# Kernel tuning notes

Hardware: AMD Instinct MI355X
Metric: run time of the kernel (lower is better)

The kernel has to match this reference:

```python
import jax, jax.numpy as jnp
import numpy as np

EMBED_DIM = 1024
NUM_HEADS = 16
HEAD_DIM = EMBED_DIM // NUM_HEADS
SCALE = HEAD_DIM ** -0.5
BATCH, SEQ = 2, 2048


def setup_inputs() -> dict:
    key = jax.random.key(0)
    k1, k2, k3 = jax.random.split(key, 3)
    # Xavier-uniform-like init scales
    s_qkv = (6.0 / (3 * EMBED_DIM + EMBED_DIM)) ** 0.5
    s_out = (6.0 / (2 * EMBED_DIM)) ** 0.5
    return {
        "x": jax.random.normal(k1, (BATCH, SEQ, EMBED_DIM), dtype=jnp.float32),
        "w_qkv": jax.random.uniform(k2, (3 * EMBED_DIM, EMBED_DIM), jnp.float32, -s_qkv, s_qkv),
        "w_out": jax.random.uniform(k3, (EMBED_DIM, EMBED_DIM), jnp.float32, -s_out, s_out),
        "bias_qkv": jnp.zeros((3 * EMBED_DIM,), jnp.float32),
        "bias_out": jnp.zeros((EMBED_DIM,), jnp.float32),
    }


def reference(x, w_qkv, w_out, bias_qkv, bias_out):
    B, S, E = x.shape
    H, D = NUM_HEADS, HEAD_DIM
    # Fused QKV projection: [B,S,3E]
    qkv = jnp.einsum('bse,fe->bsf', x, w_qkv) + bias_qkv
    q, k, v = jnp.split(qkv, 3, axis=-1)
    # [B,H,S,D]
    q = q.reshape(B, S, H, D).transpose(0, 2, 1, 3)
    k = k.reshape(B, S, H, D).transpose(0, 2, 1, 3)
    v = v.reshape(B, S, H, D).transpose(0, 2, 1, 3)
    # Scaled dot-product attention (non-causal, no mask)
    scores = jnp.einsum('bhqd,bhkd->bhqk', q, k) * SCALE
    attn = jax.nn.softmax(scores, axis=-1)
    ctx = jnp.einsum('bhqk,bhkd->bhqd', attn, v)
    ctx = ctx.transpose(0, 2, 1, 3).reshape(B, S, E)
    # Output projection
    return jnp.einsum('bse,fe->bsf', ctx, w_out) + bias_out
```

## Files before the change

### kernel.cpp

```cpp
#include <hip/hip_runtime.h>
#include <stdint.h>

#define B_ 2
#define S_ 2048
#define E_ 1024
#define H_ 16
#define D_ 64
#define QSCALE_ 0.18033688011112042f

typedef __attribute__((ext_vector_type(4))) short short4_t;
typedef __attribute__((ext_vector_type(8))) short short8;
typedef __attribute__((ext_vector_type(4))) float f32x4;
typedef __attribute__((ext_vector_type(16))) float f32x16;
typedef unsigned int u32;

__device__ __forceinline__ unsigned short f2bf(float x) {
    union { float f; u32 u; } v; v.f = x;
    u32 r = v.u + 0x7fffu + ((v.u >> 16) & 1u);
    return (unsigned short)(r >> 16);
}
__device__ __forceinline__ u32 fbits(float x) {
    union { float f; u32 u; } v; v.f = x; return v.u;
}
__device__ __forceinline__ u32 pkbf(float lo, float hi) {
    return __builtin_amdgcn_perm(fbits(hi), fbits(lo), 0x07060302u);
}

__device__ __forceinline__ f32x4 mfma16(short8 a, short8 b, f32x4 c) {
    return __builtin_amdgcn_mfma_f32_16x16x32_bf16(a, b, c, 0, 0, 0);
}
__device__ __forceinline__ f32x16 mfma32(short8 a, short8 b, f32x16 c) {
    return __builtin_amdgcn_mfma_f32_32x32x16_bf16(a, b, c, 0, 0, 0);
}

__device__ __forceinline__ void gld16(const unsigned short* g, unsigned short* l) {
    __builtin_amdgcn_global_load_lds(
        (const __attribute__((address_space(1))) u32*)g,
        (__attribute__((address_space(3))) u32*)l, 16, 0, 0);
}

__global__ __launch_bounds__(256) void cvt_kernel(
    const float* __restrict__ x, const float* __restrict__ wq,
    const float* __restrict__ wo,
    unsigned short* __restrict__ xb, unsigned short* __restrict__ wqb,
    unsigned short* __restrict__ wob)
{
    const long i8 = ((long)blockIdx.x * 256 + threadIdx.x) * 8;
    const float* src; unsigned short* dst; long off;
    if (i8 < 4194304)      { src = x;  dst = xb;  off = i8; }
    else if (i8 < 7340032) { src = wq; dst = wqb; off = i8 - 4194304; }
    else                   { src = wo; dst = wob; off = i8 - 7340032; }
    f32x4 a = *(const f32x4*)(src + off);
    f32x4 b = *(const f32x4*)(src + off + 4);
    short8 o;
    o[0] = (short)f2bf(a[0]); o[1] = (short)f2bf(a[1]);
    o[2] = (short)f2bf(a[2]); o[3] = (short)f2bf(a[3]);
    o[4] = (short)f2bf(b[0]); o[5] = (short)f2bf(b[1]);
    o[6] = (short)f2bf(b[2]); o[7] = (short)f2bf(b[3]);
    *(short8*)(dst + off) = o;
}

#define GEMM_PROLOG()                                                         \
    __shared__ __attribute__((aligned(16))) unsigned short As[128 * 32];      \
    __shared__ __attribute__((aligned(16))) unsigned short Bs[128 * 32];      \
    __shared__ float biass[128];                                              \
    const int t = threadIdx.x;                                                \
    const int m0 = blockIdx.x * 128;                                          \
    const int n0 = blockIdx.y * 128;                                          \
    const int lane = t & 63;                                                  \
    const int wv = t >> 6;                                                    \
    const int g = lane >> 4;                                                  \
    const int l15 = lane & 15;                                                \
    const int wm = (wv >> 1) * 64;                                            \
    const int wn = (wv & 1) * 64;                                             \
    const int rloc = lane >> 2;                                               \
    const int cg = (lane & 3) ^ ((lane >> 3) & 3);                            \
    const int rsw = (g ^ ((l15 >> 1) & 3)) * 8;

#define GEMM_LOOP(AP, BP)                                                     \
    f32x4 acc[4][4];                                                          \
    _Pragma("unroll")                                                         \
    for (int i = 0; i < 4; ++i)                                               \
        _Pragma("unroll")                                                     \
        for (int j = 0; j < 4; ++j)                                           \
            acc[i][j] = (f32x4){0.f, 0.f, 0.f, 0.f};                          \
    for (int kt = 0; kt < E_; kt += 32) {                                     \
        __syncthreads();                                                      \
        _Pragma("unroll")                                                     \
        for (int j = 0; j < 2; ++j) {                                         \
            const int rb = 32 * wv + 16 * j;                                  \
            gld16(AP + (m0 + rb + rloc) * E_ + kt + cg * 8, &As[rb * 32]);    \
            gld16(BP + (n0 + rb + rloc) * E_ + kt + cg * 8, &Bs[rb * 32]);    \
        }                                                                     \
        __syncthreads();                                                      \
        short8 af[4], bf[4];                                                  \
        _Pragma("unroll")                                                     \
        for (int mt = 0; mt < 4; ++mt)                                        \
            af[mt] = *(const short8*)&As[(wm + mt * 16 + l15) * 32 + rsw];    \
        _Pragma("unroll")                                                     \
        for (int nt = 0; nt < 4; ++nt)                                        \
            bf[nt] = *(const short8*)&Bs[(wn + nt * 16 + l15) * 32 + rsw];    \
        _Pragma("unroll")                                                     \
        for (int mt = 0; mt < 4; ++mt)                                        \
            _Pragma("unroll")                                                 \
            for (int nt = 0; nt < 4; ++nt)                                    \
                acc[mt][nt] = mfma16(af[mt], bf[nt], acc[mt][nt]);            \
    }

__global__ __launch_bounds__(256) void qkv_gemm_kernel(
    const unsigned short* __restrict__ x, const unsigned short* __restrict__ w,
    const float* __restrict__ bias,
    unsigned short* __restrict__ Qg, unsigned short* __restrict__ Kg,
    unsigned short* __restrict__ Vtg)
{
    GEMM_PROLOG()
    if (t < 128) biass[t] = bias[n0 + t];
    GEMM_LOOP(x, w)

#pragma unroll
    for (int mt = 0; mt < 4; ++mt) {
#pragma unroll
        for (int nt = 0; nt < 4; ++nt) {
            const int col = n0 + wn + nt * 16 + l15;
            const int which = col >> 10;
            const int cr = col & 1023;
            const int h = cr >> 6;
            const int d = cr & 63;
            const float bia = biass[col - n0];
#pragma unroll
            for (int i = 0; i < 4; ++i) {
                const int row = m0 + wm + mt * 16 + g * 4 + i;
                const int bb = row >> 11;
                const int s = row & 2047;
                const int bh = bb * H_ + h;
                const float v = acc[mt][nt][i] + bia;
                if (which == 0) {
                    Qg[(bh * S_ + s) * D_ + d] = f2bf(v * QSCALE_);
                } else if (which == 1) {
                    Kg[(bh * S_ + s) * D_ + d] = f2bf(v);
                } else {
                    Vtg[(bh * D_ + d) * S_ + s] = f2bf(v);
                }
            }
        }
    }
}

__global__ __launch_bounds__(256) void out_gemm_kernel(
    const unsigned short* __restrict__ ctxg, const unsigned short* __restrict__ w,
    const float* __restrict__ bias, float* __restrict__ out)
{
    GEMM_PROLOG()
    if (t < 128) biass[t] = bias[n0 + t];
    GEMM_LOOP(ctxg, w)

#pragma unroll
    for (int mt = 0; mt < 4; ++mt) {
#pragma unroll
        for (int nt = 0; nt < 4; ++nt) {
            const int col = n0 + wn + nt * 16 + l15;
            const float bia = biass[col - n0];
#pragma unroll
            for (int i = 0; i < 4; ++i) {
                const int row = m0 + wm + mt * 16 + g * 4 + i;
                out[row * E_ + col] = acc[mt][nt][i] + bia;
            }
        }
    }
}

__global__ __launch_bounds__(256) void attn_kernel(
    const unsigned short* __restrict__ Qg, const unsigned short* __restrict__ Kg,
    const unsigned short* __restrict__ Vtg, unsigned short* __restrict__ ctx)
{
    __shared__ __attribute__((aligned(16))) unsigned short Ks[2][64 * 64];
    __shared__ __attribute__((aligned(16))) unsigned short Vs[2][64 * 64];
    __shared__ float lsumbuf[128];

    const int t = threadIdx.x;
    const int qb = blockIdx.x;
    const int bh = blockIdx.y;
    const int bb = bh >> 4;
    const int hh = bh & 15;
    const int lane = t & 63;
    const int wv = t >> 6;
    const int l31 = lane & 31;
    const int hf = lane >> 5;
    const int rloc = lane >> 3;
    const int cg = (lane & 7) ^ ((lane >> 3) & 7);
    const int sw = (l31 & 7);

    const int qrow0 = qb * 128 + wv * 32;
    short8 qa[4];
#pragma unroll
    for (int kc = 0; kc < 4; ++kc)
        qa[kc] = *(const short8*)(Qg + (bh * S_ + qrow0 + l31) * D_ + kc * 16 + hf * 8);

    f32x16 O[2];
    float lsum = 0.f;
#pragma unroll
    for (int r = 0; r < 16; ++r) { O[0][r] = 0.f; O[1][r] = 0.f; }

    auto stage = [&](int kb2, int bufi) {
#pragma unroll
        for (int j = 0; j < 2; ++j) {
            const int rb = 16 * wv + 8 * j;
            gld16(Kg + (bh * S_ + kb2 * 64 + rb + rloc) * D_ + cg * 8, &Ks[bufi][rb * 64]);
            gld16(Vtg + (bh * D_ + rb + rloc) * S_ + kb2 * 64 + cg * 8, &Vs[bufi][rb * 64]);
        }
    };

    stage(0, 0);

    for (int kb = 0; kb < S_ / 64; ++kb) {
        __syncthreads();
        if (kb + 1 < S_ / 64) stage(kb + 1, (kb + 1) & 1);
        const unsigned short* ks = Ks[kb & 1];
        const unsigned short* vs = Vs[kb & 1];

        f32x16 st[2];
#pragma unroll
        for (int kt = 0; kt < 2; ++kt) {
            f32x16 s;
#pragma unroll
            for (int r = 0; r < 16; ++r) s[r] = 0.f;
#pragma unroll
            for (int kc = 0; kc < 4; ++kc) {
                short8 kf = *(const short8*)&ks[(kt * 32 + l31) * 64 + ((2 * kc + hf) ^ sw) * 8];
                s = mfma32(kf, qa[kc], s);
            }
            st[kt] = s;
        }

        float e[2][16];
#pragma unroll
        for (int kt = 0; kt < 2; ++kt)
#pragma unroll
            for (int r = 0; r < 16; ++r) {
                const float p = __builtin_amdgcn_exp2f(st[kt][r]);
                e[kt][r] = p;
                lsum += p;
            }

#pragma unroll
        for (int kt = 0; kt < 2; ++kt) {
#pragma unroll
            for (int cp = 0; cp < 2; ++cp) {
                union { short8 s8; u32 u[4]; } pa;
                pa.u[0] = pkbf(e[kt][8 * cp + 0], e[kt][8 * cp + 1]);
                pa.u[1] = pkbf(e[kt][8 * cp + 2], e[kt][8 * cp + 3]);
                pa.u[2] = pkbf(e[kt][8 * cp + 4], e[kt][8 * cp + 5]);
                pa.u[3] = pkbf(e[kt][8 * cp + 6], e[kt][8 * cp + 7]);
                const int c0 = ((4 * kt + 2 * cp) ^ sw) * 8 + 4 * hf;
                const int c1 = ((4 * kt + 2 * cp + 1) ^ sw) * 8 + 4 * hf;
#pragma unroll
                for (int dt = 0; dt < 2; ++dt) {
                    short4_t v0 = *(const short4_t*)&vs[(dt * 32 + l31) * 64 + c0];
                    short4_t v1 = *(const short4_t*)&vs[(dt * 32 + l31) * 64 + c1];
                    short8 vb = __builtin_shufflevector(v0, v1, 0, 1, 2, 3, 4, 5, 6, 7);
                    O[dt] = mfma32(pa.s8, vb, O[dt]);
                }
            }
        }
    }

    lsum += __shfl_xor(lsum, 32);
    if (hf == 0) lsumbuf[wv * 32 + l31] = lsum;
    float inv[16];
#pragma unroll
    for (int r = 0; r < 16; ++r) {
        const int ql = wv * 32 + 4 * hf + (r & 3) + 8 * (r >> 2);
        inv[r] = 1.0f / lsumbuf[ql];
    }

#pragma unroll
    for (int dt = 0; dt < 2; ++dt)
#pragma unroll
        for (int r = 0; r < 16; ++r) {
            const int ql = wv * 32 + 4 * hf + (r & 3) + 8 * (r >> 2);
            const int s = qb * 128 + ql;
            ctx[(bb * S_ + s) * E_ + hh * D_ + dt * 32 + l31] = f2bf(O[dt][r] * inv[r]);
        }
}

extern "C" void kernel_launch(void* const* d_in, const int* in_sizes, int n_in,
                              void* d_out, int out_size, void* d_ws, size_t ws_size,
                              hipStream_t stream) {
    const float* x    = (const float*)d_in[0];
    const float* wqkv = (const float*)d_in[1];
    const float* wout = (const float*)d_in[2];
    const float* bqkv = (const float*)d_in[3];
    const float* bout = (const float*)d_in[4];

    unsigned short* Q   = (unsigned short*)d_ws;
    unsigned short* K   = Q + 4194304;
    unsigned short* Vt  = K + 4194304;
    unsigned short* ctx = Vt + 4194304;
    unsigned short* xb  = ctx;
    unsigned short* wqb = ctx + 4194304;
    unsigned short* wob = wqb + 3145728;

    cvt_kernel<<<4096, 256, 0, stream>>>(x, wqkv, wout, xb, wqb, wob);
    qkv_gemm_kernel<<<dim3(32, 24), 256, 0, stream>>>(xb, wqb, bqkv, Q, K, Vt);
    attn_kernel<<<dim3(16, 32), 256, 0, stream>>>(Q, K, Vt, ctx);
    out_gemm_kernel<<<dim3(32, 8), 256, 0, stream>>>(ctx, wob, bout, (float*)d_out);
}
```

Before: 190.7 us.

## Transpose V through LDS, shrink attention and out-GEMM tiles for more blocks

The QKV GEMM epilogue for the V section now stages accumulators through shared memory so that V-transposed rows are written with 16-byte coalesced stores, replacing scattered 2-byte strided writes. The attention kernel moves to 64-query blocks of 128 threads with incrementally advanced load pointers, and accumulates the softmax denominator as a packed float2 fused into the exp/pack loop. The output GEMM uses 128x64 tiles, which doubles the grid. These changes aim to cut uncoalesced store traffic and raise occupancy and wave count, at the cost of extra synchronisation in the epilogue and less K/V tile reuse per attention block.

```diff
diff --git a/kernel.cpp b/kernel.cpp
--- a/kernel.cpp
+++ b/kernel.cpp
@@ -10,6 +10,7 @@
 
 typedef __attribute__((ext_vector_type(4))) short short4_t;
 typedef __attribute__((ext_vector_type(8))) short short8;
+typedef __attribute__((ext_vector_type(2))) float f32x2;
 typedef __attribute__((ext_vector_type(4))) float f32x4;
 typedef __attribute__((ext_vector_type(16))) float f32x16;
 typedef unsigned int u32;
@@ -60,122 +61,137 @@
     *(short8*)(dst + off) = o;
 }
 
-#define GEMM_PROLOG()                                                         \
-    __shared__ __attribute__((aligned(16))) unsigned short As[128 * 32];      \
-    __shared__ __attribute__((aligned(16))) unsigned short Bs[128 * 32];      \
-    __shared__ float biass[128];                                              \
-    const int t = threadIdx.x;                                                \
-    const int m0 = blockIdx.x * 128;                                          \
-    const int n0 = blockIdx.y * 128;                                          \
-    const int lane = t & 63;                                                  \
-    const int wv = t >> 6;                                                    \
-    const int g = lane >> 4;                                                  \
-    const int l15 = lane & 15;                                                \
-    const int wm = (wv >> 1) * 64;                                            \
-    const int wn = (wv & 1) * 64;                                             \
-    const int rloc = lane >> 2;                                               \
-    const int cg = (lane & 3) ^ ((lane >> 3) & 3);                            \
-    const int rsw = (g ^ ((l15 >> 1) & 3)) * 8;
-
-#define GEMM_LOOP(AP, BP)                                                     \
-    f32x4 acc[4][4];                                                          \
-    _Pragma("unroll")                                                         \
-    for (int i = 0; i < 4; ++i)                                               \
-        _Pragma("unroll")                                                     \
-        for (int j = 0; j < 4; ++j)                                           \
-            acc[i][j] = (f32x4){0.f, 0.f, 0.f, 0.f};                          \
-    for (int kt = 0; kt < E_; kt += 32) {                                     \
-        __syncthreads();                                                      \
-        _Pragma("unroll")                                                     \
-        for (int j = 0; j < 2; ++j) {                                         \
-            const int rb = 32 * wv + 16 * j;                                  \
-            gld16(AP + (m0 + rb + rloc) * E_ + kt + cg * 8, &As[rb * 32]);    \
-            gld16(BP + (n0 + rb + rloc) * E_ + kt + cg * 8, &Bs[rb * 32]);    \
-        }                                                                     \
-        __syncthreads();                                                      \
-        short8 af[4], bf[4];                                                  \
-        _Pragma("unroll")                                                     \
-        for (int mt = 0; mt < 4; ++mt)                                        \
-            af[mt] = *(const short8*)&As[(wm + mt * 16 + l15) * 32 + rsw];    \
-        _Pragma("unroll")                                                     \
-        for (int nt = 0; nt < 4; ++nt)                                        \
-            bf[nt] = *(const short8*)&Bs[(wn + nt * 16 + l15) * 32 + rsw];    \
-        _Pragma("unroll")                                                     \
-        for (int mt = 0; mt < 4; ++mt)                                        \
-            _Pragma("unroll")                                                 \
-            for (int nt = 0; nt < 4; ++nt)                                    \
-                acc[mt][nt] = mfma16(af[mt], bf[nt], acc[mt][nt]);            \
-    }
-
 __global__ __launch_bounds__(256) void qkv_gemm_kernel(
     const unsigned short* __restrict__ x, const unsigned short* __restrict__ w,
     const float* __restrict__ bias,
     unsigned short* __restrict__ Qg, unsigned short* __restrict__ Kg,
     unsigned short* __restrict__ Vtg)
 {
-    GEMM_PROLOG()
+    __shared__ __attribute__((aligned(16))) unsigned char smem[16896];
+    __shared__ float biass[128];
+    unsigned short* As = (unsigned short*)smem;
+    unsigned short* Bs = (unsigned short*)(smem + 8192);
+    float* Tr = (float*)smem;
+
+    const int t = threadIdx.x;
+    const int m0 = blockIdx.x * 128;
+    const int n0 = blockIdx.y * 128;
+    const int lane = t & 63;
+    const int wv = t >> 6;
+    const int g = lane >> 4;
+    const int l15 = lane & 15;
+    const int wm = (wv >> 1) * 64;
+    const int wn = (wv & 1) * 64;
+    const int rloc = lane >> 2;
+    const int cg = (lane & 3) ^ ((lane >> 3) & 3);
+    const int rsw = (g ^ ((l15 >> 1) & 3)) * 8;
+
     if (t < 128) biass[t] = bias[n0 + t];
-    GEMM_LOOP(x, w)
-
-#pragma unroll
-    for (int mt = 0; mt < 4; ++mt) {
-#pragma unroll
-        for (int nt = 0; nt < 4; ++nt) {
-            const int col = n0 + wn + nt * 16 + l15;
-            const int which = col >> 10;
-            const int cr = col & 1023;
-            const int h = cr >> 6;
-            const int d = cr & 63;
-            const float bia = biass[col - n0];
-#pragma unroll
-            for (int i = 0; i < 4; ++i) {
-                const int row = m0 + wm + mt * 16 + g * 4 + i;
-                const int bb = row >> 11;
-                const int s = row & 2047;
-                const int bh = bb * H_ + h;
-                const float v = acc[mt][nt][i] + bia;
-                if (which == 0) {
-                    Qg[(bh * S_ + s) * D_ + d] = f2bf(v * QSCALE_);
-                } else if (which == 1) {
-                    Kg[(bh * S_ + s) * D_ + d] = f2bf(v);
-                } else {
-                    Vtg[(bh * D_ + d) * S_ + s] = f2bf(v);
+
+    f32x4 acc[4][4];
+#pragma unroll
+    for (int i = 0; i < 4; ++i)
+#pragma unroll
+        for (int j = 0; j < 4; ++j)
+            acc[i][j] = (f32x4){0.f, 0.f, 0.f, 0.f};
+
+    for (int kt = 0; kt < E_; kt += 32) {
+        __syncthreads();
+#pragma unroll
+        for (int j = 0; j < 2; ++j) {
+            const int rb = 32 * wv + 16 * j;
+            gld16(x + (m0 + rb + rloc) * E_ + kt + cg * 8, &As[rb * 32]);
+            gld16(w + (n0 + rb + rloc) * E_ + kt + cg * 8, &Bs[rb * 32]);
+        }
+        __syncthreads();
+
+        short8 af[4], bf[4];
+#pragma unroll
+        for (int mt = 0; mt < 4; ++mt)
+            af[mt] = *(const short8*)&As[(wm + mt * 16 + l15) * 32 + rsw];
+#pragma unroll
+        for (int nt = 0; nt < 4; ++nt)
+            bf[nt] = *(const short8*)&Bs[(wn + nt * 16 + l15) * 32 + rsw];
+#pragma unroll
+        for (int mt = 0; mt < 4; ++mt)
+#pragma unroll
+            for (int nt = 0; nt < 4; ++nt)
+                acc[mt][nt] = mfma16(af[mt], bf[nt], acc[mt][nt]);
+    }
+
+    if (n0 < 2048) {
+#pragma unroll
+        for (int mt = 0; mt < 4; ++mt) {
+#pragma unroll
+            for (int nt = 0; nt < 4; ++nt) {
+                const int col = n0 + wn + nt * 16 + l15;
+                const int which = col >> 10;
+                const int cr = col & 1023;
+                const int h = cr >> 6;
+                const int d = cr & 63;
+                const float bia = biass[col - n0];
+#pragma unroll
+                for (int i = 0; i < 4; ++i) {
+                    const int row = m0 + wm + mt * 16 + g * 4 + i;
+                    const int bb = row >> 11;
+                    const int s = row & 2047;
+                    const int bh = bb * H_ + h;
+                    const float v = acc[mt][nt][i] + bia;
+                    if (which == 0)
+                        Qg[(bh * S_ + s) * D_ + d] = f2bf(v * QSCALE_);
+                    else
+                        Kg[(bh * S_ + s) * D_ + d] = f2bf(v);
                 }
             }
         }
-    }
-}
-
-__global__ __launch_bounds__(256) void out_gemm_kernel(
-    const unsigned short* __restrict__ ctxg, const unsigned short* __restrict__ w,
-    const float* __restrict__ bias, float* __restrict__ out)
-{
-    GEMM_PROLOG()
-    if (t < 128) biass[t] = bias[n0 + t];
-    GEMM_LOOP(ctxg, w)
-
-#pragma unroll
-    for (int mt = 0; mt < 4; ++mt) {
-#pragma unroll
-        for (int nt = 0; nt < 4; ++nt) {
-            const int col = n0 + wn + nt * 16 + l15;
-            const float bia = biass[col - n0];
-#pragma unroll
-            for (int i = 0; i < 4; ++i) {
-                const int row = m0 + wm + mt * 16 + g * 4 + i;
-                out[row * E_ + col] = acc[mt][nt][i] + bia;
+    } else {
+        const int bb = m0 >> 11;
+        const int s0 = m0 & 2047;
+        const int dth = t >> 3;
+        const int sc = t & 7;
+#pragma unroll
+        for (int sl = 0; sl < 4; ++sl) {
+            __syncthreads();
+            if ((wv & 1) == (sl >> 1)) {
+#pragma unroll
+                for (int q = 0; q < 2; ++q) {
+                    const int nt = (sl & 1) * 2 + q;
+                    const float bia = biass[wn + nt * 16 + l15];
+                    const int dloc = q * 16 + l15;
+#pragma unroll
+                    for (int mt = 0; mt < 4; ++mt)
+#pragma unroll
+                        for (int i = 0; i < 4; ++i)
+                            Tr[(wm + mt * 16 + g * 4 + i) * 33 + dloc] =
+                                acc[mt][nt][i] + bia;
+                }
             }
-        }
-    }
-}
-
-__global__ __launch_bounds__(256) void attn_kernel(
+            __syncthreads();
+            const int dglob = (n0 - 2048) + sl * 32 + dth;
+            const int h = dglob >> 6;
+            const int dd = dglob & 63;
+            unsigned short* dst =
+                Vtg + ((long)(bb * H_ + h) * D_ + dd) * S_ + s0 + sc * 16;
+            short8 o0, o1;
+#pragma unroll
+            for (int j = 0; j < 8; ++j)
+                o0[j] = (short)f2bf(Tr[(sc * 16 + j) * 33 + dth]);
+#pragma unroll
+            for (int j = 0; j < 8; ++j)
+                o1[j] = (short)f2bf(Tr[(sc * 16 + 8 + j) * 33 + dth]);
+            *(short8*)dst = o0;
+            *(short8*)(dst + 8) = o1;
+        }
+    }
+}
+
+__global__ __launch_bounds__(128) void attn_kernel(
     const unsigned short* __restrict__ Qg, const unsigned short* __restrict__ Kg,
     const unsigned short* __restrict__ Vtg, unsigned short* __restrict__ ctx)
 {
     __shared__ __attribute__((aligned(16))) unsigned short Ks[2][64 * 64];
     __shared__ __attribute__((aligned(16))) unsigned short Vs[2][64 * 64];
-    __shared__ float lsumbuf[128];
+    __shared__ float lsumbuf[64];
 
     const int t = threadIdx.x;
     const int qb = blockIdx.x;
@@ -190,31 +206,46 @@
     const int cg = (lane & 7) ^ ((lane >> 3) & 7);
     const int sw = (l31 & 7);
 
-    const int qrow0 = qb * 128 + wv * 32;
+    const int qrow0 = qb * 64 + wv * 32;
     short8 qa[4];
 #pragma unroll
     for (int kc = 0; kc < 4; ++kc)
         qa[kc] = *(const short8*)(Qg + (bh * S_ + qrow0 + l31) * D_ + kc * 16 + hf * 8);
 
+    const unsigned short* kp = Kg + (bh * S_ + 32 * wv + rloc) * D_ + cg * 8;
+    const unsigned short* vp0 = Vtg + ((bh * D_ + 32 * wv + 0  + rloc) * S_) + cg * 8;
+    const unsigned short* vp1 = Vtg + ((bh * D_ + 32 * wv + 8  + rloc) * S_) + cg * 8;
+    const unsigned short* vp2 = Vtg + ((bh * D_ + 32 * wv + 16 + rloc) * S_) + cg * 8;
+    const unsigned short* vp3 = Vtg + ((bh * D_ + 32 * wv + 24 + rloc) * S_) + cg * 8;
+
     f32x16 O[2];
-    float lsum = 0.f;
+    f32x2 lsum2 = (f32x2){0.f, 0.f};
 #pragma unroll
     for (int r = 0; r < 16; ++r) { O[0][r] = 0.f; O[1][r] = 0.f; }
 
-    auto stage = [&](int kb2, int bufi) {
-#pragma unroll
-        for (int j = 0; j < 2; ++j) {
-            const int rb = 16 * wv + 8 * j;
-            gld16(Kg + (bh * S_ + kb2 * 64 + rb + rloc) * D_ + cg * 8, &Ks[bufi][rb * 64]);
-            gld16(Vtg + (bh * D_ + rb + rloc) * S_ + kb2 * 64 + cg * 8, &Vs[bufi][rb * 64]);
-        }
+    auto stage = [&](int bufi) {
+        unsigned short* kd = &Ks[bufi][(32 * wv) * 64];
+        unsigned short* vd = &Vs[bufi][(32 * wv) * 64];
+        gld16(kp,        kd);
+        gld16(kp + 512,  kd + 512);
+        gld16(kp + 1024, kd + 1024);
+        gld16(kp + 1536, kd + 1536);
+        gld16(vp0, vd);
+        gld16(vp1, vd + 512);
+        gld16(vp2, vd + 1024);
+        gld16(vp3, vd + 1536);
     };
-
-    stage(0, 0);
+    auto advance = [&]() {
+        kp += 64 * D_;
+        vp0 += 64; vp1 += 64; vp2 += 64; vp3 += 64;
+    };
+
+    stage(0);
+    advance();
 
     for (int kb = 0; kb < S_ / 64; ++kb) {
         __syncthreads();
-        if (kb + 1 < S_ / 64) stage(kb + 1, (kb + 1) & 1);
+        if (kb + 1 < S_ / 64) { stage((kb + 1) & 1); advance(); }
         const unsigned short* ks = Ks[kb & 1];
         const unsigned short* vs = Vs[kb & 1];
 
@@ -232,25 +263,23 @@
             st[kt] = s;
         }
 
-        float e[2][16];
-#pragma unroll
-        for (int kt = 0; kt < 2; ++kt)
-#pragma unroll
-            for (int r = 0; r < 16; ++r) {
-                const float p = __builtin_amdgcn_exp2f(st[kt][r]);
-                e[kt][r] = p;
-                lsum += p;
-            }
-
 #pragma unroll
         for (int kt = 0; kt < 2; ++kt) {
 #pragma unroll
             for (int cp = 0; cp < 2; ++cp) {
+                float p[8];
+#pragma unroll
+                for (int j = 0; j < 8; ++j)
+                    p[j] = __builtin_amdgcn_exp2f(st[kt][8 * cp + j]);
+                lsum2 += (f32x2){p[0], p[1]};
+                lsum2 += (f32x2){p[2], p[3]};
+                lsum2 += (f32x2){p[4], p[5]};
+                lsum2 += (f32x2){p[6], p[7]};
                 union { short8 s8; u32 u[4]; } pa;
-                pa.u[0] = pkbf(e[kt][8 * cp + 0], e[kt][8 * cp + 1]);
-                pa.u[1] = pkbf(e[kt][8 * cp + 2], e[kt][8 * cp + 3]);
-                pa.u[2] = pkbf(e[kt][8 * cp + 4], e[kt][8 * cp + 5]);
-                pa.u[3] = pkbf(e[kt][8 * cp + 6], e[kt][8 * cp + 7]);
+                pa.u[0] = pkbf(p[0], p[1]);
+                pa.u[1] = pkbf(p[2], p[3]);
+                pa.u[2] = pkbf(p[4], p[5]);
+                pa.u[3] = pkbf(p[6], p[7]);
                 const int c0 = ((4 * kt + 2 * cp) ^ sw) * 8 + 4 * hf;
                 const int c1 = ((4 * kt + 2 * cp + 1) ^ sw) * 8 + 4 * hf;
 #pragma unroll
@@ -264,6 +293,7 @@
         }
     }
 
+    float lsum = lsum2[0] + lsum2[1];
     lsum += __shfl_xor(lsum, 32);
     if (hf == 0) lsumbuf[wv * 32 + l31] = lsum;
     float inv[16];
@@ -278,9 +308,81 @@
 #pragma unroll
         for (int r = 0; r < 16; ++r) {
             const int ql = wv * 32 + 4 * hf + (r & 3) + 8 * (r >> 2);
-            const int s = qb * 128 + ql;
+            const int s = qb * 64 + ql;
             ctx[(bb * S_ + s) * E_ + hh * D_ + dt * 32 + l31] = f2bf(O[dt][r] * inv[r]);
         }
+}
+
+__global__ __launch_bounds__(256) void out_gemm_kernel(
+    const unsigned short* __restrict__ ctxg, const unsigned short* __restrict__ w,
+    const float* __restrict__ bias, float* __restrict__ out)
+{
+    __shared__ __attribute__((aligned(16))) unsigned short As[128 * 32];
+    __shared__ __attribute__((aligned(16))) unsigned short Bs[64 * 32];
+    __shared__ float biass[64];
+
+    const int t = threadIdx.x;
+    const int m0 = blockIdx.x * 128;
+    const int n0 = blockIdx.y * 64;
+    const int lane = t & 63;
+    const int wv = t >> 6;
+    const int g = lane >> 4;
+    const int l15 = lane & 15;
+    const int wm = (wv >> 1) * 64;
+    const int wn = (wv & 1) * 32;
+    const int rloc = lane >> 2;
+    const int cg = (lane & 3) ^ ((lane >> 3) & 3);
+    const int rsw = (g ^ ((l15 >> 1) & 3)) * 8;
+
+    if (t < 64) biass[t] = bias[n0 + t];
+
+    f32x4 acc[4][2];
+#pragma unroll
+    for (int i = 0; i < 4; ++i)
+#pragma unroll
+        for (int j = 0; j < 2; ++j)
+            acc[i][j] = (f32x4){0.f, 0.f, 0.f, 0.f};
+
+    for (int kt = 0; kt < E_; kt += 32) {
+        __syncthreads();
+#pragma unroll
+        for (int j = 0; j < 2; ++j) {
+            const int rb = 32 * wv + 16 * j;
+            gld16(ctxg + (m0 + rb + rloc) * E_ + kt + cg * 8, &As[rb * 32]);
+        }
+        {
+            const int rb = 16 * wv;
+            gld16(w + (n0 + rb + rloc) * E_ + kt + cg * 8, &Bs[rb * 32]);
+        }
+        __syncthreads();
+
+        short8 af[4], bf[2];
+#pragma unroll
+        for (int mt = 0; mt < 4; ++mt)
+            af[mt] = *(const short8*)&As[(wm + mt * 16 + l15) * 32 + rsw];
+#pragma unroll
+        for (int nt = 0; nt < 2; ++nt)
+            bf[nt] = *(const short8*)&Bs[(wn + nt * 16 + l15) * 32 + rsw];
+#pragma unroll
+        for (int mt = 0; mt < 4; ++mt)
+#pragma unroll
+            for (int nt = 0; nt < 2; ++nt)
+                acc[mt][nt] = mfma16(af[mt], bf[nt], acc[mt][nt]);
+    }
+
+#pragma unroll
+    for (int mt = 0; mt < 4; ++mt) {
+#pragma unroll
+        for (int nt = 0; nt < 2; ++nt) {
+            const int col = n0 + wn + nt * 16 + l15;
+            const float bia = biass[col - n0];
+#pragma unroll
+            for (int i = 0; i < 4; ++i) {
+                const int row = m0 + wm + mt * 16 + g * 4 + i;
+                out[row * E_ + col] = acc[mt][nt][i] + bia;
+            }
+        }
+    }
 }
 
 extern "C" void kernel_launch(void* const* d_in, const int* in_sizes, int n_in,
@@ -302,6 +404,6 @@
 
     cvt_kernel<<<4096, 256, 0, stream>>>(x, wqkv, wout, xb, wqb, wob);
     qkv_gemm_kernel<<<dim3(32, 24), 256, 0, stream>>>(xb, wqb, bqkv, Q, K, Vt);
-    attn_kernel<<<dim3(16, 32), 256, 0, stream>>>(Q, K, Vt, ctx);
-    out_gemm_kernel<<<dim3(32, 8), 256, 0, stream>>>(ctx, wob, bout, (float*)d_out);
-}
+    attn_kernel<<<dim3(32, 32), 128, 0, stream>>>(Q, K, Vt, ctx);
+    out_gemm_kernel<<<dim3(32, 16), 256, 0, stream>>>(ctx, wob, bout, (float*)d_out);
+}
```

Result: no change. 188.2 us (-1.3%).
